# Optimization experiments

Measured on AMD Instinct MI355X. Metric: run time of the kernel, lower is better.

The kernel has to match this reference:

```python
import jax, jax.numpy as jnp
import numpy as np

B, T, HIDDEN, CQ, CKV, NH, HD, RD = 4, 4096, 4096, 1536, 512, 32, 128, 64


def _rope(x):
    # x: (b, s, n, r); positions = arange(s) (decode step gets pos 0, matching
    # the module which passes no offset to RotaryPositionEmbedding)
    s, r = x.shape[1], x.shape[-1]
    inv_freq = 1.0 / (10000.0 ** (jnp.arange(0, r, 2, dtype=jnp.float32) / r))
    ang = jnp.arange(s, dtype=jnp.float32)[:, None] * inv_freq[None, :]  # (s, r/2)
    cos = jnp.cos(ang)[None, :, None, :].astype(x.dtype)
    sin = jnp.sin(ang)[None, :, None, :].astype(x.dtype)
    x1, x2 = x[..., ::2], x[..., 1::2]
    return jnp.stack([x1 * cos - x2 * sin, x1 * sin + x2 * cos], axis=-1).reshape(x.shape)


def setup_inputs() -> dict:
    key = jax.random.key(0)
    ks = jax.random.split(key, 12)
    wscale = jnp.float32(0.02)
    return {
        "hidden_states": jax.random.normal(ks[0], (B, 1, HIDDEN), jnp.float32),
        "mask": jnp.zeros((B, 1, NH, T + 1), jnp.float32),
        "cached_cKV": jax.random.normal(ks[1], (B, T, CKV), jnp.float32),
        "cached_kR": jax.random.normal(ks[2], (B, T, NH, RD), jnp.float32),
        "W_DQ": jax.random.normal(ks[3], (HIDDEN, CQ), jnp.float32) * wscale,
        "W_DKV": jax.random.normal(ks[4], (HIDDEN, CKV), jnp.float32) * wscale,
        "W_UQ_C": jax.random.normal(ks[5], (CQ, NH, HD), jnp.float32) * wscale,
        "W_UQ_R": jax.random.normal(ks[6], (CQ, NH, RD), jnp.float32) * wscale,
        "W_UK_C": jax.random.normal(ks[7], (CKV, NH, HD), jnp.float32) * wscale,
        "W_UV_C": jax.random.normal(ks[8], (CKV, NH, HD), jnp.float32) * wscale,
        "W_KR": jax.random.normal(ks[9], (HIDDEN, NH, RD), jnp.float32) * wscale,
        "W_O": jax.random.normal(ks[10], (NH, HD, HIDDEN), jnp.float32) * wscale,
    }


def reference(hidden_states, mask, cached_cKV, cached_kR,
              W_DQ, W_DKV, W_UQ_C, W_UQ_R, W_UK_C, W_UV_C, W_KR, W_O):
    Bc = hidden_states.shape[0]
    # query path
    cQ_t = jnp.einsum('bsh,hq->bsq', hidden_states, W_DQ)
    qC_t = jnp.einsum('bsq,qnd->bsnd', cQ_t, W_UQ_C)
    qR_t = jnp.einsum('bsq,qnr->bsnr', cQ_t, W_UQ_R)
    kR_t_raw = jnp.einsum('bsh,hnr->bsnr', hidden_states, W_KR)
    qR_t = _rope(qR_t)
    kR_t = _rope(kR_t_raw)
    # compressed KV for the new token
    cKV_t = jnp.einsum('bsh,hv->bsv', hidden_states, W_DKV)
    kC_t = jnp.einsum('bsv,vnd->bsnd', cKV_t, W_UK_C)
    vC_t = jnp.einsum('bsv,vnd->bsnd', cKV_t, W_UV_C)
    # decompress prefix cache and score
    prefix_len = cached_cKV.shape[1]
    kC_prefix = jnp.einsum('btv,vnd->btnd', cached_cKV, W_UK_C)   # (B,T,n,d)
    prefix_scores = (jnp.einsum('bsnd,btnd->bsnt', qC_t, kC_prefix)
                     + jnp.einsum('bsnr,btnr->bsnt', qR_t, cached_kR))
    new_score = (jnp.einsum('bsnd,bsnd->bsn', qC_t, kC_t)
                 + jnp.einsum('bsnr,bsnr->bsn', qR_t, kR_t))[..., None]
    attn_scores = jnp.concatenate([prefix_scores, new_score], axis=-1)
    scale = jnp.sqrt(jnp.float32(HD + RD)).astype(attn_scores.dtype)
    attn_scores = attn_scores / scale
    if mask is not None:
        attn_scores = attn_scores + mask * jnp.asarray(-1e9, attn_scores.dtype)
    attn_probs = jax.nn.softmax(attn_scores, axis=-1)
    # value aggregation
    vC_prefix = jnp.einsum('btv,vnd->btnd', cached_cKV, W_UV_C)
    prefix_agg = jnp.einsum('bsnt,btnd->bsnd', attn_probs[..., :prefix_len], vC_prefix)
    new_agg = attn_probs[..., -1:].reshape(Bc, 1, NH, 1) * vC_t
    attn_out = prefix_agg + new_agg
    output = jnp.einsum('bsnd,ndh->bsh', attn_out, W_O)
    new_cached_cKV = jnp.concatenate([cached_cKV, cKV_t], axis=1)
    new_cached_kR = jnp.concatenate([cached_kR, kR_t], axis=1)
    return (output, new_cached_cKV, new_cached_kR)
```

## Files before the change

kernel.cpp:

```cpp
#include <hip/hip_runtime.h>

#define TT 4096
#define T1 4097

using f32x4 = __attribute__((ext_vector_type(4))) float;

__device__ __forceinline__ void gemv_body(const float* __restrict__ X,
                                          const float* __restrict__ W,
                                          float* __restrict__ Y,
                                          int N, int K, int chunk, int ky) {
  const int tid = threadIdx.x;
  const int ct = tid & 7;
  const int kt = tid >> 3;
  const int col0 = blockIdx.x * 32 + ct * 4;
  const int k0 = ky * chunk;
  float acc[4][4];
#pragma unroll
  for (int c = 0; c < 4; ++c)
#pragma unroll
    for (int b = 0; b < 4; ++b) acc[c][b] = 0.f;
  const int iters = chunk >> 5;
  for (int i = 0; i < iters; ++i) {
    int k = k0 + kt + (i << 5);
    f32x4 w4 = *(const f32x4*)(W + (size_t)k * N + col0);
    float xb[4];
#pragma unroll
    for (int b = 0; b < 4; ++b) xb[b] = X[(size_t)b * K + k];
#pragma unroll
    for (int c = 0; c < 4; ++c)
#pragma unroll
      for (int b = 0; b < 4; ++b) acc[c][b] += w4[c] * xb[b];
  }
  __shared__ float red[256][16];
#pragma unroll
  for (int c = 0; c < 4; ++c)
#pragma unroll
    for (int b = 0; b < 4; ++b) red[tid][c * 4 + b] = acc[c][b];
  __syncthreads();
  for (int s = 16; s >= 1; s >>= 1) {
    if (kt < s) {
#pragma unroll
      for (int j = 0; j < 16; ++j) red[tid][j] += red[tid + 8 * s][j];
    }
    __syncthreads();
  }
  if (kt == 0) {
#pragma unroll
    for (int c = 0; c < 4; ++c)
#pragma unroll
      for (int b = 0; b < 4; ++b)
        atomicAdd(&Y[(size_t)b * N + col0 + c], red[ct][c * 4 + b]);
  }
}

__global__ __launch_bounds__(256) void gemv_hidden(const float* __restrict__ X,
                                                   const float* __restrict__ W0,
                                                   const float* __restrict__ W1,
                                                   const float* __restrict__ W2,
                                                   float* __restrict__ Ybase) {
  const int z = blockIdx.z;
  const float* W = (z == 0) ? W0 : (z == 1) ? W1 : W2;
  const int N = (z == 0) ? 1536 : (z == 1) ? 512 : 2048;
  const int nb = (z == 0) ? 48 : (z == 1) ? 16 : 64;
  const size_t yoff = (z == 0) ? 0 : (z == 1) ? 6144 : 8192;
  if ((int)blockIdx.x >= nb) return;
  gemv_body(X, W, Ybase + yoff, N, 4096, 512, blockIdx.y);
}

__global__ __launch_bounds__(256) void gemv_cq(const float* __restrict__ X,
                                               const float* __restrict__ W0,
                                               const float* __restrict__ W1,
                                               float* __restrict__ Y0,
                                               float* __restrict__ Y1) {
  const int z = blockIdx.z;
  const float* W = (z == 0) ? W0 : W1;
  float* Y = (z == 0) ? Y0 : Y1;
  const int N = (z == 0) ? 4096 : 2048;
  const int nb = (z == 0) ? 128 : 64;
  if ((int)blockIdx.x >= nb) return;
  gemv_body(X, W, Y, N, 1536, 384, blockIdx.y);
}

__global__ __launch_bounds__(256) void gemv_atomic(const float* __restrict__ X,
                                                   const float* __restrict__ W,
                                                   float* __restrict__ Y,
                                                   int N, int K, int chunk) {
  gemv_body(X, W, Y, N, K, chunk, blockIdx.y);
}

__global__ __launch_bounds__(128) void absorb_kernel(const float* __restrict__ qC,
                                                     const float* __restrict__ W_UK,
                                                     float* __restrict__ q_abs,
                                                     float* __restrict__ qT) {
  const int n = blockIdx.x, vt = blockIdx.y;
  __shared__ float qs[4][128];
  for (int i = threadIdx.x; i < 512; i += 128)
    qs[i >> 7][i & 127] = qC[(size_t)(i >> 7) * 4096 + n * 128 + (i & 127)];
  __syncthreads();
  const int v = vt * 128 + threadIdx.x;
  const float* wp = W_UK + (size_t)v * 4096 + n * 128;
  float acc[4] = {0.f, 0.f, 0.f, 0.f};
#pragma unroll 8
  for (int c = 0; c < 32; ++c) {
    f32x4 w4 = *(const f32x4*)(wp + c * 4);
#pragma unroll
    for (int j = 0; j < 4; ++j)
#pragma unroll
      for (int b = 0; b < 4; ++b) acc[b] += qs[b][c * 4 + j] * w4[j];
  }
#pragma unroll
  for (int b = 0; b < 4; ++b) {
    q_abs[((size_t)(b * 32) + n) * 512 + v] = acc[b];
    qT[((size_t)b * 512 + v) * 32 + n] = acc[b];
  }
}

__global__ __launch_bounds__(256, 4) void scores_split(const float* __restrict__ cKV,
                                                       const float* __restrict__ kR,
                                                       const float* __restrict__ qT,
                                                       const float* __restrict__ qR,
                                                       float* __restrict__ scores,
                                                       float* __restrict__ scoresR,
                                                       float* __restrict__ out_ckv,
                                                       float* __restrict__ out_kr) {
  const int bid = blockIdx.x;
  const int idx = bid >> 1;
  const int tid = threadIdx.x;
  const int b = idx >> 9;
  const int t0 = (idx & 511) * 8;
  __shared__ float ck[8][516];
  if (bid & 1) {
    for (int i = tid; i < 1024; i += 256) {
      int tl = i >> 7, vq = i & 127;
      f32x4 v = *(const f32x4*)(cKV + ((size_t)b * TT + t0 + tl) * 512 + vq * 4);
      *(f32x4*)&ck[tl][vq * 4] = v;
      *(f32x4*)(out_ckv + ((size_t)b * T1 + t0 + tl) * 512 + vq * 4) = v;
    }
    __syncthreads();
    const int tl = tid >> 5, n = tid & 31;
    const float* qtb = qT + (size_t)b * 16384 + n;
    float a = 0.f;
#pragma unroll 8
    for (int v = 0; v < 512; ++v) a += qtb[(size_t)v * 32] * ck[tl][v];
    scores[((size_t)(b * 32) + n) * T1 + t0 + tl] = a;
  } else {
    const int w = tid >> 6, l = tid & 63;
    f32x4 q[8];
#pragma unroll
    for (int k = 0; k < 8; ++k)
      q[k] = *(const f32x4*)(qR + (size_t)b * 2048 + l * 4 + k * 256);
    const int nbase = l >> 4;
    const int wlead = ((l & 15) == 0);
#pragma unroll
    for (int r = 0; r < 2; ++r) {
      const int t = t0 + w * 2 + r;
      const float* src = kR + ((size_t)b * TT + t) * 2048 + l * 4;
      float* dst = out_kr + ((size_t)b * T1 + t) * 2048 + l * 4;
      f32x4 v[8];
#pragma unroll
      for (int k = 0; k < 8; ++k) v[k] = *(const f32x4*)(src + k * 256);
#pragma unroll
      for (int k = 0; k < 8; ++k) *(f32x4*)(dst + k * 256) = v[k];
      float p[8];
#pragma unroll
      for (int k = 0; k < 8; ++k)
        p[k] = (q[k][0] * v[k][0] + q[k][1] * v[k][1]) +
               (q[k][2] * v[k][2] + q[k][3] * v[k][3]);
#pragma unroll
      for (int k = 0; k < 8; ++k) {
        p[k] += __shfl_xor(p[k], 1);
        p[k] += __shfl_xor(p[k], 2);
        p[k] += __shfl_xor(p[k], 4);
        p[k] += __shfl_xor(p[k], 8);
      }
      if (wlead) {
#pragma unroll
        for (int k = 0; k < 8; ++k)
          scoresR[((size_t)(b * 32) + k * 4 + nbase) * T1 + t] = p[k];
      }
    }
  }
}

__global__ __launch_bounds__(256) void softmax_kernel(float* __restrict__ scores,
                                                      const float* __restrict__ scoresR,
                                                      const float* __restrict__ mask,
                                                      const float* __restrict__ q_abs,
                                                      const float* __restrict__ cKV_t,
                                                      const float* __restrict__ qR,
                                                      const float* __restrict__ kR_t) {
  const int b = blockIdx.x >> 5, n = blockIdx.x & 31;
  const int tid = threadIdx.x;
  float* srow = scores + ((size_t)(b * 32) + n) * T1;
  const float* scrow = scoresR + ((size_t)(b * 32) + n) * T1;
  const float* qa = q_abs + ((size_t)(b * 32) + n) * 512;
  const float* ck = cKV_t + b * 512;
  float p = qa[tid] * ck[tid] + qa[tid + 256] * ck[tid + 256];
  if (tid < 64) p += qR[(size_t)b * 2048 + n * 64 + tid] * kR_t[(size_t)b * 2048 + n * 64 + tid];
  __shared__ float lds[256];
  lds[tid] = p;
  __syncthreads();
  for (int s = 128; s >= 1; s >>= 1) {
    if (tid < s) lds[tid] += lds[tid + s];
    __syncthreads();
  }
  const float sT = lds[0];
  __syncthreads();
  const float inv_scale = 0.0721687836487032f;
  const float* mrow = mask + ((size_t)(b * 32) + n) * T1;
  float lmax = -1e30f;
  for (int t = tid; t < T1; t += 256) {
    float s0 = (t < TT) ? (srow[t] + scrow[t]) : sT;
    float val = s0 * inv_scale + mrow[t] * (-1e9f);
    srow[t] = val;
    lmax = fmaxf(lmax, val);
  }
  lds[tid] = lmax;
  __syncthreads();
  for (int s = 128; s >= 1; s >>= 1) {
    if (tid < s) lds[tid] = fmaxf(lds[tid], lds[tid + s]);
    __syncthreads();
  }
  const float M = lds[0];
  __syncthreads();
  float lsum = 0.f;
  for (int t = tid; t < T1; t += 256) {
    float e = expf(srow[t] - M);
    srow[t] = e;
    lsum += e;
  }
  lds[tid] = lsum;
  __syncthreads();
  for (int s = 128; s >= 1; s >>= 1) {
    if (tid < s) lds[tid] += lds[tid + s];
    __syncthreads();
  }
  const float inv = 1.0f / lds[0];
  for (int t = tid; t < T1; t += 256) srow[t] *= inv;
}

__global__ __launch_bounds__(256) void agg_part(const float* __restrict__ cKV,
                                                const float* __restrict__ probs,
                                                float* __restrict__ aggP,
                                                int tlen, int NC) {
  const int chunk = blockIdx.x, b = blockIdx.y, vh = blockIdx.z;
  const int tid = threadIdx.x;
  const int vg = tid & 31, ng = tid >> 5;
  __shared__ float p_lds[32 * 129];
  float acc[4][4];
#pragma unroll
  for (int a = 0; a < 4; ++a)
#pragma unroll
    for (int j = 0; j < 4; ++j) acc[a][j] = 0.f;
  const int sub = (tlen < 128) ? tlen : 128;
  const int sshift = (sub == 64) ? 6 : 7;
  for (int tt = 0; tt < tlen; tt += sub) {
    const int t0 = chunk * tlen + tt;
    __syncthreads();
    for (int i = tid; i < (sub << 5); i += 256) {
      int n = i >> sshift, tl = i & (sub - 1);
      p_lds[n * 129 + tl] = probs[((size_t)(b * 32) + n) * T1 + t0 + tl];
    }
    __syncthreads();
    const float* cbase = cKV + ((size_t)b * TT + t0) * 512 + vh * 128 + vg * 4;
    for (int t = 0; t < sub; t += 2) {
      f32x4 c0 = *(const f32x4*)(cbase + (size_t)t * 512);
      f32x4 c1 = *(const f32x4*)(cbase + (size_t)(t + 1) * 512);
#pragma unroll
      for (int a = 0; a < 4; ++a) {
        float p0 = p_lds[(ng * 4 + a) * 129 + t];
        float p1 = p_lds[(ng * 4 + a) * 129 + t + 1];
#pragma unroll
        for (int j = 0; j < 4; ++j) acc[a][j] += p0 * c0[j] + p1 * c1[j];
      }
    }
  }
#pragma unroll
  for (int a = 0; a < 4; ++a) {
    int n = ng * 4 + a;
    float* dst = aggP + (((size_t)b * NC + chunk) * 32 + n) * 512 + vh * 128 + vg * 4;
    f32x4 v;
#pragma unroll
    for (int j = 0; j < 4; ++j) v[j] = acc[a][j];
    *(f32x4*)dst = v;
  }
}

__global__ __launch_bounds__(256) void agg_reduce(const float* __restrict__ aggP,
                                                  const float* __restrict__ probs,
                                                  const float* __restrict__ cKV_t,
                                                  float* __restrict__ agg, int NC) {
  const int idx = blockIdx.x * 256 + threadIdx.x;
  const int b = idx >> 14;
  const int n = (idx >> 9) & 31;
  const int v = idx & 511;
  float s = probs[((size_t)(b * 32) + n) * T1 + TT] * cKV_t[b * 512 + v];
  const float* pp = aggP + (((size_t)b * NC) * 32 + n) * 512 + v;
#pragma unroll 4
  for (int c = 0; c < NC; ++c) s += pp[(size_t)c * 32 * 512];
  agg[idx] = s;
}

__global__ __launch_bounds__(256) void out1_kernel(const float* __restrict__ agg,
                                                   const float* __restrict__ W_UV,
                                                   float* __restrict__ attn_out) {
  const int n = blockIdx.x, vc = blockIdx.y;
  const int tid = threadIdx.x;
  const int d = tid & 127, bh = tid >> 7;
  const float* a0 = agg + ((size_t)(bh * 32) + n) * 512;
  const float* a1 = agg + ((size_t)((bh + 2) * 32) + n) * 512;
  float acc0 = 0.f, acc1 = 0.f;
#pragma unroll 4
  for (int vv = 0; vv < 64; ++vv) {
    int v = vc * 64 + vv;
    float w = W_UV[(size_t)v * 4096 + n * 128 + d];
    acc0 += a0[v] * w;
    acc1 += a1[v] * w;
  }
  atomicAdd(&attn_out[(size_t)bh * 4096 + n * 128 + d], acc0);
  atomicAdd(&attn_out[(size_t)(bh + 2) * 4096 + n * 128 + d], acc1);
}

__global__ __launch_bounds__(256) void finalize_kernel(const float* __restrict__ outf,
                                                       const float* __restrict__ cKV_t,
                                                       const float* __restrict__ kR_t,
                                                       float* __restrict__ out) {
  int idx = blockIdx.x * 256 + threadIdx.x;
  if (idx < 16384) {
    out[idx] = outf[idx];
    return;
  }
  idx -= 16384;
  if (idx < 2048) {
    int b = idx >> 9, v = idx & 511;
    out[16384 + ((size_t)b * T1 + TT) * 512 + v] = cKV_t[idx];
    return;
  }
  idx -= 2048;
  if (idx < 8192) {
    int b = idx >> 11;
    int c = idx & 2047;
    out[16384 + (size_t)8390656 + ((size_t)b * T1 + TT) * 2048 + c] = kR_t[idx];
  }
}

extern "C" void kernel_launch(void* const* d_in, const int* in_sizes, int n_in,
                              void* d_out, int out_size, void* d_ws, size_t ws_size,
                              hipStream_t stream) {
  (void)in_sizes; (void)n_in; (void)out_size;
  const float* hidden = (const float*)d_in[0];
  const float* mask   = (const float*)d_in[1];
  const float* cKV    = (const float*)d_in[2];
  const float* kR     = (const float*)d_in[3];
  const float* W_DQ   = (const float*)d_in[4];
  const float* W_DKV  = (const float*)d_in[5];
  const float* W_UQ_C = (const float*)d_in[6];
  const float* W_UQ_R = (const float*)d_in[7];
  const float* W_UK_C = (const float*)d_in[8];
  const float* W_UV_C = (const float*)d_in[9];
  const float* W_KR   = (const float*)d_in[10];
  const float* W_O    = (const float*)d_in[11];

  float* ws = (float*)d_ws;
  const size_t WS_CQ = 0;
  const size_t WS_CKVT = 6144;
  const size_t WS_KRT = 8192;
  const size_t WS_QC = 16384;
  const size_t WS_QR = 32768;
  const size_t WS_OUTF = 40960;
  const size_t WS_ATTN = 57344;
  const size_t WS_AGG = 73728;
  const size_t WS_QABS = 139264;
  const size_t WS_SCORES = 204800;
  const size_t WS_QT = 729216;
  const size_t WS_SCR = 794752;
  const size_t WS_AGGP = 1319168;

  int NC = 8;
  if (ws_size >= (WS_AGGP + (size_t)64 * 65536) * 4) NC = 64;
  else if (ws_size >= (WS_AGGP + (size_t)32 * 65536) * 4) NC = 32;
  else if (ws_size >= (WS_AGGP + (size_t)16 * 65536) * 4) NC = 16;
  const int tlen = 4096 / NC;

  float* out0 = (float*)d_out;
  float* out_ckv = out0 + 16384;
  float* out_kr = out_ckv + (size_t)8390656;

  hipMemsetAsync(d_ws, 0, 73728 * sizeof(float), stream);

  gemv_hidden<<<dim3(64, 8, 3), 256, 0, stream>>>(hidden, W_DQ, W_DKV, W_KR, ws);
  gemv_cq<<<dim3(128, 4, 2), 256, 0, stream>>>(ws + WS_CQ, W_UQ_C, W_UQ_R,
                                               ws + WS_QC, ws + WS_QR);
  absorb_kernel<<<dim3(32, 4), 128, 0, stream>>>(ws + WS_QC, W_UK_C, ws + WS_QABS, ws + WS_QT);
  scores_split<<<4096, 256, 0, stream>>>(cKV, kR, ws + WS_QT, ws + WS_QR,
                                         ws + WS_SCORES, ws + WS_SCR, out_ckv, out_kr);
  softmax_kernel<<<128, 256, 0, stream>>>(ws + WS_SCORES, ws + WS_SCR, mask, ws + WS_QABS,
                                          ws + WS_CKVT, ws + WS_QR, ws + WS_KRT);
  agg_part<<<dim3(NC, 4, 4), 256, 0, stream>>>(cKV, ws + WS_SCORES, ws + WS_AGGP,
                                               tlen, NC);
  agg_reduce<<<256, 256, 0, stream>>>(ws + WS_AGGP, ws + WS_SCORES, ws + WS_CKVT,
                                      ws + WS_AGG, NC);
  out1_kernel<<<dim3(32, 8), 256, 0, stream>>>(ws + WS_AGG, W_UV_C, ws + WS_ATTN);
  gemv_atomic<<<dim3(128, 8), 256, 0, stream>>>(ws + WS_ATTN, W_O, ws + WS_OUTF, 4096, 4096, 512);
  finalize_kernel<<<104, 256, 0, stream>>>(ws + WS_OUTF, ws + WS_CKVT, ws + WS_KRT, out0);
}
```

Before: 223.9 us.

## Use online softmax stats and recompute probabilities in aggregation; nontemporal cache copies

The softmax kernel now computes only per-row max and inverse-sum in a single online pass and writes them to a small stats buffer, rather than making three passes that write normalized probabilities back into the scores array. The aggregation kernel recomputes each probability on the fly from the raw scores, rope scores, mask and stats. This removes two read/write sweeps over the score rows but adds exp work and extra loads in agg_part, which is run across 4 value-slice blocks and so repeats the recomputation. The KV-cache copy stores in the scores kernel also switch to nontemporal stores to reduce cache pollution.

```diff
diff --git a/kernel.cpp b/kernel.cpp
--- a/kernel.cpp
+++ b/kernel.cpp
@@ -134,7 +134,7 @@
       int tl = i >> 7, vq = i & 127;
       f32x4 v = *(const f32x4*)(cKV + ((size_t)b * TT + t0 + tl) * 512 + vq * 4);
       *(f32x4*)&ck[tl][vq * 4] = v;
-      *(f32x4*)(out_ckv + ((size_t)b * T1 + t0 + tl) * 512 + vq * 4) = v;
+      __builtin_nontemporal_store(v, (f32x4*)(out_ckv + ((size_t)b * T1 + t0 + tl) * 512 + vq * 4));
     }
     __syncthreads();
     const int tl = tid >> 5, n = tid & 31;
@@ -160,7 +160,8 @@
 #pragma unroll
       for (int k = 0; k < 8; ++k) v[k] = *(const f32x4*)(src + k * 256);
 #pragma unroll
-      for (int k = 0; k < 8; ++k) *(f32x4*)(dst + k * 256) = v[k];
+      for (int k = 0; k < 8; ++k)
+        __builtin_nontemporal_store(v[k], (f32x4*)(dst + k * 256));
       float p[8];
 #pragma unroll
       for (int k = 0; k < 8; ++k)
@@ -182,18 +183,21 @@
   }
 }
 
-__global__ __launch_bounds__(256) void softmax_kernel(float* __restrict__ scores,
-                                                      const float* __restrict__ scoresR,
-                                                      const float* __restrict__ mask,
-                                                      const float* __restrict__ q_abs,
-                                                      const float* __restrict__ cKV_t,
-                                                      const float* __restrict__ qR,
-                                                      const float* __restrict__ kR_t) {
+__global__ __launch_bounds__(256) void softmax_stats(const float* __restrict__ scores,
+                                                     const float* __restrict__ scoresR,
+                                                     const float* __restrict__ mask,
+                                                     const float* __restrict__ q_abs,
+                                                     const float* __restrict__ cKV_t,
+                                                     const float* __restrict__ qR,
+                                                     const float* __restrict__ kR_t,
+                                                     float* __restrict__ stats) {
   const int b = blockIdx.x >> 5, n = blockIdx.x & 31;
   const int tid = threadIdx.x;
-  float* srow = scores + ((size_t)(b * 32) + n) * T1;
-  const float* scrow = scoresR + ((size_t)(b * 32) + n) * T1;
-  const float* qa = q_abs + ((size_t)(b * 32) + n) * 512;
+  const size_t row = (size_t)(b * 32) + n;
+  const float* srow = scores + row * T1;
+  const float* scrow = scoresR + row * T1;
+  const float* mrow = mask + row * T1;
+  const float* qa = q_abs + row * 512;
   const float* ck = cKV_t + b * 512;
   float p = qa[tid] * ck[tid] + qa[tid + 256] * ck[tid + 256];
   if (tid < 64) p += qR[(size_t)b * 2048 + n * 64 + tid] * kR_t[(size_t)b * 2048 + n * 64 + tid];
@@ -206,46 +210,51 @@
   }
   const float sT = lds[0];
   __syncthreads();
-  const float inv_scale = 0.0721687836487032f;
-  const float* mrow = mask + ((size_t)(b * 32) + n) * T1;
-  float lmax = -1e30f;
-  for (int t = tid; t < T1; t += 256) {
-    float s0 = (t < TT) ? (srow[t] + scrow[t]) : sT;
-    float val = s0 * inv_scale + mrow[t] * (-1e9f);
-    srow[t] = val;
-    lmax = fmaxf(lmax, val);
-  }
-  lds[tid] = lmax;
+  const float isc = 0.0721687836487032f;
+  float m = -1e30f, s = 0.f;
+  for (int t = tid; t < TT; t += 256) {
+    float val = (srow[t] + scrow[t]) * isc + mrow[t] * (-1e9f);
+    if (val > m) {
+      s = s * expf(m - val) + 1.f;
+      m = val;
+    } else {
+      s += expf(val - m);
+    }
+  }
+  __shared__ float lm[256], lsm[256];
+  lm[tid] = m;
+  lsm[tid] = s;
   __syncthreads();
-  for (int s = 128; s >= 1; s >>= 1) {
-    if (tid < s) lds[tid] = fmaxf(lds[tid], lds[tid + s]);
-    __syncthreads();
-  }
-  const float M = lds[0];
-  __syncthreads();
-  float lsum = 0.f;
-  for (int t = tid; t < T1; t += 256) {
-    float e = expf(srow[t] - M);
-    srow[t] = e;
-    lsum += e;
-  }
-  lds[tid] = lsum;
-  __syncthreads();
-  for (int s = 128; s >= 1; s >>= 1) {
-    if (tid < s) lds[tid] += lds[tid + s];
-    __syncthreads();
-  }
-  const float inv = 1.0f / lds[0];
-  for (int t = tid; t < T1; t += 256) srow[t] *= inv;
+  for (int st = 128; st >= 1; st >>= 1) {
+    if (tid < st) {
+      float m2 = lm[tid + st], s2 = lsm[tid + st];
+      float M = fmaxf(lm[tid], m2);
+      lsm[tid] = lsm[tid] * expf(lm[tid] - M) + s2 * expf(m2 - M);
+      lm[tid] = M;
+    }
+    __syncthreads();
+  }
+  if (tid == 0) {
+    float valT = sT * isc + mrow[TT] * (-1e9f);
+    float M = fmaxf(lm[0], valT);
+    float S = lsm[0] * expf(lm[0] - M) + expf(valT - M);
+    stats[blockIdx.x * 4 + 0] = M;
+    stats[blockIdx.x * 4 + 1] = 1.f / S;
+    stats[blockIdx.x * 4 + 2] = expf(valT - M) / S;
+  }
 }
 
 __global__ __launch_bounds__(256) void agg_part(const float* __restrict__ cKV,
-                                                const float* __restrict__ probs,
+                                                const float* __restrict__ scores,
+                                                const float* __restrict__ scoresR,
+                                                const float* __restrict__ mask,
+                                                const float* __restrict__ stats,
                                                 float* __restrict__ aggP,
                                                 int tlen, int NC) {
   const int chunk = blockIdx.x, b = blockIdx.y, vh = blockIdx.z;
   const int tid = threadIdx.x;
   const int vg = tid & 31, ng = tid >> 5;
+  const float isc = 0.0721687836487032f;
   __shared__ float p_lds[32 * 129];
   float acc[4][4];
 #pragma unroll
@@ -258,8 +267,11 @@
     const int t0 = chunk * tlen + tt;
     __syncthreads();
     for (int i = tid; i < (sub << 5); i += 256) {
-      int n = i >> sshift, tl = i & (sub - 1);
-      p_lds[n * 129 + tl] = probs[((size_t)(b * 32) + n) * T1 + t0 + tl];
+      int nn = i >> sshift, tl = i & (sub - 1);
+      size_t row = (size_t)(b * 32) + nn;
+      size_t off = row * T1 + t0 + tl;
+      float val = (scores[off] + scoresR[off]) * isc + mask[off] * (-1e9f);
+      p_lds[nn * 129 + tl] = expf(val - stats[row * 4]) * stats[row * 4 + 1];
     }
     __syncthreads();
     const float* cbase = cKV + ((size_t)b * TT + t0) * 512 + vh * 128 + vg * 4;
@@ -287,14 +299,14 @@
 }
 
 __global__ __launch_bounds__(256) void agg_reduce(const float* __restrict__ aggP,
-                                                  const float* __restrict__ probs,
+                                                  const float* __restrict__ stats,
                                                   const float* __restrict__ cKV_t,
                                                   float* __restrict__ agg, int NC) {
   const int idx = blockIdx.x * 256 + threadIdx.x;
   const int b = idx >> 14;
   const int n = (idx >> 9) & 31;
   const int v = idx & 511;
-  float s = probs[((size_t)(b * 32) + n) * T1 + TT] * cKV_t[b * 512 + v];
+  float s = stats[((size_t)(b * 32) + n) * 4 + 2] * cKV_t[b * 512 + v];
   const float* pp = aggP + (((size_t)b * NC) * 32 + n) * 512 + v;
 #pragma unroll 4
   for (int c = 0; c < NC; ++c) s += pp[(size_t)c * 32 * 512];
@@ -369,12 +381,13 @@
   const size_t WS_QR = 32768;
   const size_t WS_OUTF = 40960;
   const size_t WS_ATTN = 57344;
-  const size_t WS_AGG = 73728;
-  const size_t WS_QABS = 139264;
-  const size_t WS_SCORES = 204800;
-  const size_t WS_QT = 729216;
-  const size_t WS_SCR = 794752;
-  const size_t WS_AGGP = 1319168;
+  const size_t WS_STATS = 73728;
+  const size_t WS_AGG = 74240;
+  const size_t WS_QABS = 139776;
+  const size_t WS_QT = 205312;
+  const size_t WS_SCORES = 270848;
+  const size_t WS_SCR = 795264;
+  const size_t WS_AGGP = 1319680;
 
   int NC = 8;
   if (ws_size >= (WS_AGGP + (size_t)64 * 65536) * 4) NC = 64;
@@ -394,11 +407,11 @@
   absorb_kernel<<<dim3(32, 4), 128, 0, stream>>>(ws + WS_QC, W_UK_C, ws + WS_QABS, ws + WS_QT);
   scores_split<<<4096, 256, 0, stream>>>(cKV, kR, ws + WS_QT, ws + WS_QR,
                                          ws + WS_SCORES, ws + WS_SCR, out_ckv, out_kr);
-  softmax_kernel<<<128, 256, 0, stream>>>(ws + WS_SCORES, ws + WS_SCR, mask, ws + WS_QABS,
-                                          ws + WS_CKVT, ws + WS_QR, ws + WS_KRT);
-  agg_part<<<dim3(NC, 4, 4), 256, 0, stream>>>(cKV, ws + WS_SCORES, ws + WS_AGGP,
-                                               tlen, NC);
-  agg_reduce<<<256, 256, 0, stream>>>(ws + WS_AGGP, ws + WS_SCORES, ws + WS_CKVT,
+  softmax_stats<<<128, 256, 0, stream>>>(ws + WS_SCORES, ws + WS_SCR, mask, ws + WS_QABS,
+                                         ws + WS_CKVT, ws + WS_QR, ws + WS_KRT, ws + WS_STATS);
+  agg_part<<<dim3(NC, 4, 4), 256, 0, stream>>>(cKV, ws + WS_SCORES, ws + WS_SCR, mask,
+                                               ws + WS_STATS, ws + WS_AGGP, tlen, NC);
+  agg_reduce<<<256, 256, 0, stream>>>(ws + WS_AGGP, ws + WS_STATS, ws + WS_CKVT,
                                       ws + WS_AGG, NC);
   out1_kernel<<<dim3(32, 8), 256, 0, stream>>>(ws + WS_AGG, W_UV_C, ws + WS_ATTN);
   gemv_atomic<<<dim3(128, 8), 256, 0, stream>>>(ws + WS_ATTN, W_O, ws + WS_OUTF, 4096, 4096, 512);
```

Result: faster. 199.6 us, median of 2 (-10.9%).
